# Optimization experiments

Hardware: AMD Instinct MI355X
Metric: run time of the kernel (lower is better)

## Reference

```python
import math
import jax, jax.numpy as jnp
import numpy as np
from jax.scipy.special import xlogy, gammaln

WINDOW = 256  # window_size from init_kwargs


def get_positional_embed(seq_len, feature_size):
    # Enformer-style relative positional features; feature_size % 6 == 0.
    distances = jnp.arange(-seq_len + 1, seq_len, dtype=jnp.float32)  # (2W-1,)
    nb = feature_size // 6
    absd = jnp.abs(distances)[:, None]  # (2W-1, 1)
    # exponential basis
    max_range = math.log(seq_len) / math.log(2.0)
    half_life = 2.0 ** jnp.linspace(3.0, max_range, nb)
    feat_exp = jnp.exp(-math.log(2.0) / half_life[None, :] * absd)
    # central mask basis
    center_widths = 2.0 ** jnp.arange(1, nb + 1, dtype=jnp.float32) - 1.0
    feat_cm = (center_widths[None, :] > absd).astype(jnp.float32)
    # gamma pdf basis
    stddev = seq_len / (2.0 * nb)
    start_mean = seq_len / nb
    mean = jnp.linspace(start_mean, float(seq_len), nb)[None, :]
    concentration = (mean / stddev) ** 2
    rate = mean / stddev ** 2
    log_unnorm = xlogy(concentration - 1.0, absd) - rate * absd
    log_norm = gammaln(concentration) - concentration * jnp.log(rate)
    prob = jnp.exp(log_unnorm - log_norm) + 1e-8
    feat_gamma = prob / jnp.max(prob, axis=-1, keepdims=True)
    emb = jnp.concatenate([feat_exp, feat_cm, feat_gamma], axis=-1)
    return jnp.concatenate([emb, jnp.sign(distances)[:, None] * emb], axis=-1)  # (2W-1, F)


def relative_shift_swin(x):
    # x: (b, h, nw, t1, t2) with t2 = 2*t1 - 1  ->  (b, h, nw, t1, t1)
    b, h, w, t1, t2 = x.shape
    x = jnp.pad(x, ((0, 0), (0, 0), (0, 0), (0, 0), (1, 0)))  # pad zero at front of last dim
    x = x.reshape(b, h, w, t2 + 1, t1)
    x = x[:, :, :, 1:, :].reshape(b, h, w, t1, t2)
    return x[..., :(t2 + 1) // 2]


def setup_inputs() -> dict:
    key = jax.random.key(0)
    ks = jax.random.split(key, 7)
    B, N, C, H, D = 2, 8192, 768, 12, 64
    return {
        "x": jax.random.normal(ks[0], (B, N, C), jnp.float32),
        "w_qkv": jax.random.normal(ks[1], (C, 3 * H * D), jnp.float32) * 0.02,
        "w_out": jax.random.normal(ks[2], (H * D, C), jnp.float32) * 0.02,
        "b_out": jnp.zeros((C,), jnp.float32),
        "w_rel": jax.random.normal(ks[3], (C, H * D), jnp.float32) * 0.02,
        "rel_content_bias": jax.random.normal(ks[4], (1, H, 1, 1, D), jnp.float32),
        "rel_pos_bias": jax.random.normal(ks[5], (1, H, 1, 1, D), jnp.float32),
    }


def reference(x, w_qkv, w_out, b_out, w_rel, rel_content_bias, rel_pos_bias):
    b, n, c = x.shape
    H, D = rel_content_bias.shape[1], rel_content_bias.shape[-1]
    W = WINDOW
    nw = n // W  # n divisible by W (no padding branch)
    # qkv projection; output layout of to_qkv is (h, d, k) per 'b n (h d k) -> k b h n d'
    qkv = (x @ w_qkv).reshape(b, n, H, D, 3)
    q = jnp.transpose(qkv[..., 0], (0, 2, 1, 3)).reshape(b, H, nw, W, D)
    k = jnp.transpose(qkv[..., 1], (0, 2, 1, 3)).reshape(b, H, nw, W, D)
    v = jnp.transpose(qkv[..., 2], (0, 2, 1, 3)).reshape(b, H, nw, W, D)
    # relative position keys: 'n (h d) -> h n d'
    F = w_rel.shape[0]
    positions = get_positional_embed(W, F)  # (2W-1, F)
    rel_k = jnp.transpose((positions @ w_rel).reshape(2 * W - 1, H, D), (1, 0, 2))  # (H, 2W-1, D)
    # content attention (scaled); position attention (unscaled, as in source)
    content_attn = jnp.einsum('bhwid,bhwjd->bhwij', q + rel_content_bias, k) * (D ** -0.5)
    rel_logits = jnp.einsum('bhwid,hjd->bhwij', q + rel_pos_bias, rel_k)  # (b,H,nw,W,2W-1)
    position_attn = relative_shift_swin(rel_logits)  # (b,H,nw,W,W)
    attn = jax.nn.softmax(content_attn + position_attn, axis=-1)
    out = jnp.einsum('bhwij,bhwjd->bhwid', attn, v)  # (b,H,nw,W,D)
    out = jnp.transpose(out, (0, 2, 3, 1, 4)).reshape(b, nw, W, H * D)  # 'b h w n d -> b w n (h d)'
    out = out @ w_out + b_out
    return out.reshape(b, n, c)
```

## Files before the change

kernel.cpp:

```cpp
#include <hip/hip_runtime.h>
#include <math.h>

typedef __attribute__((ext_vector_type(8))) short bf8;
typedef __attribute__((ext_vector_type(4))) float f4;
typedef __attribute__((ext_vector_type(2))) unsigned u2;
typedef __attribute__((ext_vector_type(4))) unsigned u4;

__device__ __forceinline__ float bf2f(short s) {
    union { unsigned u; float f; } v; v.u = ((unsigned)(unsigned short)s) << 16; return v.f;
}
__device__ __forceinline__ short f2bf(float f) {
    return (short)((__float_as_uint(f) + 0x8000u) >> 16);
}
__device__ __forceinline__ unsigned pk2(float a, float b) {
    unsigned ua = __float_as_uint(a) + 0x8000u;
    unsigned ub = __float_as_uint(b) + 0x8000u;
    return __builtin_amdgcn_perm(ub, ua, 0x07060302u);
}
__device__ __forceinline__ void gload16(const short* g, short* l) {
    __builtin_amdgcn_global_load_lds(
        (const __attribute__((address_space(1))) void*)g,
        (__attribute__((address_space(3))) void*)l,
        16, 0, 0);
}

__global__ __launch_bounds__(256) void xb_k(const float* __restrict__ X, short* __restrict__ XB) {
    long idx = (long)blockIdx.x * 256 + threadIdx.x;
    const float* src = X + idx * 8;
    float4 v0 = *(const float4*)(src);
    float4 v1 = *(const float4*)(src + 4);
    u4 p; p.x = pk2(v0.x, v0.y); p.y = pk2(v0.z, v0.w);
    p.z = pk2(v1.x, v1.y); p.w = pk2(v1.z, v1.w);
    *(u4*)(XB + idx * 8) = p;
}

__global__ void pos_kernel(short* __restrict__ P) {
    const int row = blockIdx.x;
    const int j = threadIdx.x;
    if (row == 511) {
        for (int t = j; t < 768; t += 128) P[511 * 768 + t] = 0;
        return;
    }
    const double dist = (double)(row - 255);
    const double ad = fabs(dist);
    double hl = exp2(3.0 + 5.0 * (double)j / 127.0);
    double fe = exp(-M_LN2 / hl * ad);
    double cw = exp2((double)(j + 1)) - 1.0;
    double fc = (cw > ad) ? 1.0 : 0.0;
    double m = 2.0 + 2.0 * (double)j;
    double conc = m * m;
    double lun = (ad == 0.0) ? -INFINITY : (conc - 1.0) * log(ad);
    lun -= m * ad;
    double lnorm = lgamma(conc) - conc * log(m);
    double prob = exp(lun - lnorm) + 1e-8;
    __shared__ double red[128];
    red[j] = prob;
    __syncthreads();
    for (int s2 = 64; s2 > 0; s2 >>= 1) {
        if (j < s2) red[j] = fmax(red[j], red[j + s2]);
        __syncthreads();
    }
    double fg = prob / red[0];
    float sg = (dist > 0.0) ? 1.f : ((dist < 0.0) ? -1.f : 0.f);
    int base = row * 768;
    P[base + j]        = f2bf((float)fe);
    P[base + 128 + j]  = f2bf((float)fc);
    P[base + 256 + j]  = f2bf((float)fg);
    P[base + 384 + j]  = f2bf(sg * (float)fe);
    P[base + 512 + j]  = f2bf(sg * (float)fc);
    P[base + 640 + j]  = f2bf(sg * (float)fg);
}

__global__ void wT_k(const float* __restrict__ W, short* __restrict__ WT,
                     int K, int N, int qperm) {
    int idx = blockIdx.x * 256 + threadIdx.x;
    int kq = K >> 2;
    if (idx >= N * kq) return;
    int n = idx / kq, k = (idx % kq) << 2;
    int rp = n;
    if (qperm) { int sel = n % 3, hd = n / 3; rp = sel * 768 + hd; }
    float a = W[(long)(k + 0) * N + n];
    float b = W[(long)(k + 1) * N + n];
    float c = W[(long)(k + 2) * N + n];
    float d = W[(long)(k + 3) * N + n];
    u2 r; r.x = pk2(a, b); r.y = pk2(c, d);
    *(u2*)(WT + (long)rp * K + k) = r;
}

__global__ __launch_bounds__(256) void gemm_k(
    const short* __restrict__ A, const short* __restrict__ BT,
    int M, int N, int K, int mode,
    short* __restrict__ Cb, float* __restrict__ Cf, const float* __restrict__ bias,
    short* __restrict__ Qo, short* __restrict__ Ko, short* __restrict__ Vt)
{
    __shared__ __attribute__((aligned(16))) short lds[2][8192];
    const int tid = threadIdx.x;
    const int lane = tid & 63;
    const int wave = tid >> 6;
    const int wm = wave >> 1, wn = wave & 1;
    const int c = lane & 15, quad = lane >> 4;
    const int m0 = blockIdx.x * 128, n0 = blockIdx.y * 128;
    const int lrow = lane >> 2;
    const int lslot = lane & 3;

    f4 acc[4][4];
#pragma unroll
    for (int i = 0; i < 4; ++i)
#pragma unroll
        for (int jx = 0; jx < 4; ++jx) acc[i][jx] = (f4){0.f, 0.f, 0.f, 0.f};

    const int nT = K >> 5;

    auto stage = [&](int buf, int k0) {
        short* As = &lds[buf][0];
        short* Bs = &lds[buf][4096];
#pragma unroll
        for (int i = 0; i < 2; ++i) {
            int grp = wave * 2 + i;
            int row = grp * 16 + lrow;
            int ss = lslot ^ ((row >> 1) & 3);
            const short* srcA;
            if (mode == 2) {
                int m = m0 + row;
                srcA = A + (((long)((m >> 13) * 12 + (k0 >> 6)) * 8192 + (m & 8191)) * 64
                            + (k0 & 63) + ss * 8);
            } else {
                srcA = A + (long)(m0 + row) * K + k0 + ss * 8;
            }
            gload16(srcA, &As[grp * 512]);
            const short* srcB = BT + (long)(n0 + row) * K + k0 + ss * 8;
            gload16(srcB, &Bs[grp * 512]);
        }
    };

    stage(0, 0);
    __syncthreads();

    for (int t = 0, cur = 0; t < nT; ++t, cur ^= 1) {
        if (t + 1 < nT) stage(cur ^ 1, (t + 1) << 5);
        const short* As = &lds[cur][0];
        const short* Bs = &lds[cur][4096];
        bf8 a[4], b[4];
#pragma unroll
        for (int mt = 0; mt < 4; ++mt) {
            int row = wm * 64 + mt * 16 + c;
            int slot = quad ^ ((row >> 1) & 3);
            a[mt] = *(const bf8*)(&As[row * 32 + slot * 8]);
        }
#pragma unroll
        for (int nt = 0; nt < 4; ++nt) {
            int row = wn * 64 + nt * 16 + c;
            int slot = quad ^ ((row >> 1) & 3);
            b[nt] = *(const bf8*)(&Bs[row * 32 + slot * 8]);
        }
#pragma unroll
        for (int mt = 0; mt < 4; ++mt)
#pragma unroll
            for (int nt = 0; nt < 4; ++nt)
                acc[mt][nt] = __builtin_amdgcn_mfma_f32_16x16x32_bf16(a[mt], b[nt], acc[mt][nt], 0, 0, 0);
        __syncthreads();
    }

    if (mode == 1) {
        const int sel = n0 / 768;
        if (sel == 2) {
#pragma unroll
            for (int mt = 0; mt < 4; ++mt)
#pragma unroll
                for (int nt = 0; nt < 4; ++nt)
#pragma unroll
                    for (int r = 0; r < 4; ++r) {
                        int m = m0 + wm * 64 + mt * 16 + quad * 4 + r;
                        int np = n0 - 1536 + wn * 64 + nt * 16 + c;
                        int h = np >> 6, d = np & 63;
                        int bb = m >> 13, nn = m & 8191;
                        long off = ((long)((bb * 12 + h) * 32 + (nn >> 8))) * 16384 + d * 256 + (nn & 255);
                        Vt[off] = f2bf(acc[mt][nt][r]);
                    }
        } else {
            short* dst = (sel == 0) ? Qo : Ko;
            const int nb = n0 - sel * 768;
#pragma unroll
            for (int mt = 0; mt < 4; ++mt)
#pragma unroll
                for (int nt = 0; nt < 4; ++nt)
#pragma unroll
                    for (int r = 0; r < 4; ++r) {
                        int m = m0 + wm * 64 + mt * 16 + quad * 4 + r;
                        int np = nb + wn * 64 + nt * 16 + c;
                        int h = np >> 6, d = np & 63;
                        int bb = m >> 13, nn = m & 8191;
                        long off = ((long)((bb * 12 + h) * 8192 + nn)) * 64 + d;
                        dst[off] = f2bf(acc[mt][nt][r]);
                    }
        }
    } else {
#pragma unroll
        for (int mt = 0; mt < 4; ++mt)
#pragma unroll
            for (int nt = 0; nt < 4; ++nt)
#pragma unroll
                for (int r = 0; r < 4; ++r) {
                    int m = m0 + wm * 64 + mt * 16 + quad * 4 + r;
                    int n = n0 + wn * 64 + nt * 16 + c;
                    float val = acc[mt][nt][r];
                    if (mode == 2) {
                        Cf[(long)m * N + n] = val + bias[n];
                    } else {
                        Cb[(long)m * N + n] = f2bf(val);
                    }
                }
    }
}

__global__ __launch_bounds__(256) void attn_k(
    short* __restrict__ Q, const short* __restrict__ Kk, const short* __restrict__ Vt,
    const short* __restrict__ RK,
    const float* __restrict__ rcb, const float* __restrict__ rpb)
{
    __shared__ __attribute__((aligned(16))) short Ks[256 * 64];
    __shared__ __attribute__((aligned(16))) short Ps[4][16 * 36];
    const int bid = blockIdx.x;
    const int low = bid & 7;
    const int wlo = low >> 1;
    const int hlo = low & 1;
    const int rest = bid >> 3;
    const int strip = rest & 3;
    const int t_ = rest >> 2;
    const int whi = t_ & 7;
    const int u_ = t_ >> 3;
    const int h = ((u_ % 6) << 1) | hlo;
    const int b = u_ / 6;
    const int w = (whi << 2) | wlo;
    const int tid = threadIdx.x, lane = tid & 63, wave = tid >> 6;
    const int c = lane & 15, quad = lane >> 4;
    const int i0w = strip * 64 + wave * 16;

    const long base_bh = ((long)(b * 12 + h) * 8192 + (long)w * 256) * 64;
    short* Qh = Q + base_bh;
    const short* Kh = Kk + base_bh;
    const short* Vw = Vt + (((long)(b * 12 + h) * 32 + w) << 14);
    const short* RKh = RK + h * 64;

#pragma unroll
    for (int i = 0; i < 8; ++i) {
        int p = tid + i * 256;
        int row = p >> 3, ls = p & 7;
        gload16(Kh + row * 64 + (ls ^ (row & 7)) * 8, &Ks[(wave * 64 + i * 256) * 8]);
    }

    bf8 qc[2], qp[2];
#pragma unroll
    for (int ks = 0; ks < 2; ++ks) {
        bf8 qraw = *(const bf8*)(Qh + (i0w + c) * 64 + ks * 32 + quad * 8);
        float4 cb0 = *(const float4*)(rcb + h * 64 + ks * 32 + quad * 8);
        float4 cb1 = *(const float4*)(rcb + h * 64 + ks * 32 + quad * 8 + 4);
        float4 pb0 = *(const float4*)(rpb + h * 64 + ks * 32 + quad * 8);
        float4 pb1 = *(const float4*)(rpb + h * 64 + ks * 32 + quad * 8 + 4);
        float cbv[8] = {cb0.x, cb0.y, cb0.z, cb0.w, cb1.x, cb1.y, cb1.z, cb1.w};
        float pbv[8] = {pb0.x, pb0.y, pb0.z, pb0.w, pb1.x, pb1.y, pb1.z, pb1.w};
#pragma unroll
        for (int u = 0; u < 8; ++u) {
            float qv = bf2f(qraw[u]);
            qc[ks][u] = f2bf(qv + cbv[u]);
            qp[ks][u] = f2bf(qv + pbv[u]);
        }
    }
    __syncthreads();

    f4 S[16];
#pragma unroll
    for (int ct = 0; ct < 16; ++ct) S[ct] = (f4){0.f, 0.f, 0.f, 0.f};
#pragma unroll
    for (int t = 0; t < 16; ++t) {
        int row = t * 16 + c;
#pragma unroll
        for (int ks = 0; ks < 2; ++ks) {
            bf8 kf = *(const bf8*)(&Ks[row * 64 + (((ks * 4 + quad) ^ (row & 7))) * 8]);
            S[t] = __builtin_amdgcn_mfma_f32_16x16x32_bf16(qc[ks], kf, S[t], 0, 0, 0);
        }
    }
    __syncthreads();

    short* Vs = Ks;
#pragma unroll
    for (int i = 0; i < 8; ++i) {
        int p = tid + i * 256;
        int row = p >> 5, ls = p & 31;
        gload16(Vw + row * 256 + (ls ^ ((row & 7) << 2)) * 8, &Vs[(wave * 2 + i * 8) * 256]);
    }

    const int r0 = 240 - i0w;
    int src_[4];
#pragma unroll
    for (int r = 0; r < 4; ++r) {
        int ip = quad * 4 + r;
        src_[r] = (lane & 48) | ((15 - ip + c) & 15);
    }
    float rotp[4], rotc[4];
#pragma unroll
    for (int t = 0; t < 17; ++t) {
        bf8 rf0 = *(const bf8*)(RKh + (long)(r0 + t * 16 + c) * 768 + quad * 8);
        bf8 rf1 = *(const bf8*)(RKh + (long)(r0 + t * 16 + c) * 768 + 32 + quad * 8);
        f4 Rt = (f4){0.f, 0.f, 0.f, 0.f};
        Rt = __builtin_amdgcn_mfma_f32_16x16x32_bf16(qp[0], rf0, Rt, 0, 0, 0);
        Rt = __builtin_amdgcn_mfma_f32_16x16x32_bf16(qp[1], rf1, Rt, 0, 0, 0);
#pragma unroll
        for (int r = 0; r < 4; ++r) rotc[r] = __shfl(Rt[r], src_[r]);
        if (t > 0) {
#pragma unroll
            for (int r = 0; r < 4; ++r) {
                int ip = quad * 4 + r;
                float pos = (c <= ip) ? rotp[r] : rotc[r];
                S[t - 1][r] = S[t - 1][r] * 0.125f + pos;
            }
        }
#pragma unroll
        for (int r = 0; r < 4; ++r) rotp[r] = rotc[r];
    }

    float mx[4] = {-3.4e38f, -3.4e38f, -3.4e38f, -3.4e38f};
#pragma unroll
    for (int ct = 0; ct < 16; ++ct)
#pragma unroll
        for (int r = 0; r < 4; ++r) mx[r] = fmaxf(mx[r], S[ct][r]);
#pragma unroll
    for (int r = 0; r < 4; ++r)
#pragma unroll
        for (int o = 1; o < 16; o <<= 1) mx[r] = fmaxf(mx[r], __shfl_xor(mx[r], o));
    float sm[4] = {0.f, 0.f, 0.f, 0.f};
#pragma unroll
    for (int ct = 0; ct < 16; ++ct)
#pragma unroll
        for (int r = 0; r < 4; ++r) {
            float p = __expf(S[ct][r] - mx[r]);
            S[ct][r] = p;
            sm[r] += p;
        }
#pragma unroll
    for (int r = 0; r < 4; ++r)
#pragma unroll
        for (int o = 1; o < 16; o <<= 1) sm[r] += __shfl_xor(sm[r], o);
    float inv[4];
#pragma unroll
    for (int r = 0; r < 4; ++r) inv[r] = 1.0f / sm[r];

    __syncthreads();

    f4 O[4];
#pragma unroll
    for (int vt = 0; vt < 4; ++vt) O[vt] = (f4){0.f, 0.f, 0.f, 0.f};
#pragma unroll
    for (int kt = 0; kt < 8; ++kt) {
#pragma unroll
        for (int r = 0; r < 4; ++r) {
            Ps[wave][(quad * 4 + r) * 36 + c]      = f2bf(S[kt * 2][r] * inv[r]);
            Ps[wave][(quad * 4 + r) * 36 + 16 + c] = f2bf(S[kt * 2 + 1][r] * inv[r]);
        }
        bf8 af = *(const bf8*)(&Ps[wave][c * 36 + quad * 8]);
#pragma unroll
        for (int vt = 0; vt < 4; ++vt) {
            int row = vt * 16 + c;
            int slot = ((kt * 4 + quad) ^ ((row & 7) << 2));
            bf8 bv = *(const bf8*)(&Vs[row * 256 + slot * 8]);
            O[vt] = __builtin_amdgcn_mfma_f32_16x16x32_bf16(af, bv, O[vt], 0, 0, 0);
        }
    }
#pragma unroll
    for (int vt = 0; vt < 4; ++vt)
#pragma unroll
        for (int r = 0; r < 4; ++r)
            Qh[(i0w + quad * 4 + r) * 64 + vt * 16 + c] = f2bf(O[vt][r]);
}

extern "C" void kernel_launch(void* const* d_in, const int* in_sizes, int n_in,
                              void* d_out, int out_size, void* d_ws, size_t ws_size,
                              hipStream_t stream) {
    const float* x     = (const float*)d_in[0];
    const float* w_qkv = (const float*)d_in[1];
    const float* w_out = (const float*)d_in[2];
    const float* b_out = (const float*)d_in[3];
    const float* w_rel = (const float*)d_in[4];
    const float* rcb   = (const float*)d_in[5];
    const float* rpb   = (const float*)d_in[6];

    char* ws = (char*)d_ws;
    short* wqkvT = (short*)(ws);
    short* woutT = (short*)(ws + 3538944L);
    short* wrelT = (short*)(ws + 4718592L);
    short* pos   = (short*)(ws + 5898240L);
    short* relk  = (short*)(ws + 6684672L);
    short* q     = (short*)(ws + 7471104L);
    short* k     = (short*)(ws + 32636928L);
    short* vT    = (short*)(ws + 57802752L);
    short* xb    = (short*)d_out;

    wT_k<<<(2304 * 192 + 255) / 256, 256, 0, stream>>>(w_qkv, wqkvT, 768, 2304, 1);
    wT_k<<<(768 * 192 + 255) / 256, 256, 0, stream>>>(w_out, woutT, 768, 768, 0);
    wT_k<<<(768 * 192 + 255) / 256, 256, 0, stream>>>(w_rel, wrelT, 768, 768, 0);
    pos_kernel<<<512, 128, 0, stream>>>(pos);
    xb_k<<<6144, 256, 0, stream>>>(x, xb);
    gemm_k<<<dim3(4, 6), 256, 0, stream>>>(pos, wrelT, 512, 768, 768, 0,
                                           relk, nullptr, nullptr, nullptr, nullptr, nullptr);
    gemm_k<<<dim3(128, 18), 256, 0, stream>>>(xb, wqkvT, 16384, 2304, 768, 1,
                                              nullptr, nullptr, nullptr, q, k, vT);
    attn_k<<<3072, 256, 0, stream>>>(q, k, vT, relk, rcb, rpb);
    gemm_k<<<dim3(128, 6), 256, 0, stream>>>(q, woutT, 16384, 768, 768, 2,
                                             nullptr, (float*)d_out, b_out, nullptr, nullptr, nullptr);
}
```

Baseline: 332.3 us.

## Add 256x256-tile 8-wave GEMM with 4-stage async LDS pipeline for QKV/out projections

Introduces a new GEMM kernel with 512 threads and 256x256 output tiles, each wave computing 128x64. It uses a 4-slot LDS ring filled by direct global-to-LDS loads with explicit vmcnt waits and raised priority around the MFMA block. Both the QKV and output projections switch to it. The intent is more operand reuse and less load latency exposure, at the cost of 128KB of LDS per block (likely one block per CU) and fewer blocks to spread across CUs.

```diff
diff --git a/kernel.cpp b/kernel.cpp
--- a/kernel.cpp
+++ b/kernel.cpp
@@ -161,16 +161,114 @@
         __syncthreads();
     }
 
+#pragma unroll
+    for (int mt = 0; mt < 4; ++mt)
+#pragma unroll
+        for (int nt = 0; nt < 4; ++nt)
+#pragma unroll
+            for (int r = 0; r < 4; ++r) {
+                int m = m0 + wm * 64 + mt * 16 + quad * 4 + r;
+                int n = n0 + wn * 64 + nt * 16 + c;
+                float val = acc[mt][nt][r];
+                if (mode == 2) {
+                    Cf[(long)m * N + n] = val + bias[n];
+                } else {
+                    Cb[(long)m * N + n] = f2bf(val);
+                }
+            }
+}
+
+__global__ __launch_bounds__(512) void gemm8_k(
+    const short* __restrict__ A, const short* __restrict__ BT,
+    int M, int N, int K, int mode,
+    float* __restrict__ Cf, const float* __restrict__ bias,
+    short* __restrict__ Qo, short* __restrict__ Ko, short* __restrict__ Vt)
+{
+    __shared__ __attribute__((aligned(16))) short L[4][16384];
+    const int tid = threadIdx.x;
+    const int lane = tid & 63;
+    const int wave = tid >> 6;
+    const int wm = wave >> 2, wn = wave & 3;
+    const int c = lane & 15, quad = lane >> 4;
+    const int m0 = blockIdx.x * 256, n0 = blockIdx.y * 256;
+    const int lrow = lane >> 2;
+    const int lslot = lane & 3;
+
+    f4 acc[8][4];
+#pragma unroll
+    for (int i = 0; i < 8; ++i)
+#pragma unroll
+        for (int jx = 0; jx < 4; ++jx) acc[i][jx] = (f4){0.f, 0.f, 0.f, 0.f};
+
+    const int nT = K >> 5;
+
+    auto stage = [&](int t) {
+        int slot = t & 3;
+        int k0 = t << 5;
+#pragma unroll
+        for (int i = 0; i < 2; ++i) {
+            int row = i * 128 + wave * 16 + lrow;
+            int ss = lslot ^ ((row >> 1) & 3);
+            const short* srcA;
+            if (mode == 2) {
+                int m = m0 + row;
+                srcA = A + (((long)((m >> 13) * 12 + (k0 >> 6)) * 8192 + (m & 8191)) * 64
+                            + (k0 & 63) + ss * 8);
+            } else {
+                srcA = A + (long)(m0 + row) * K + k0 + ss * 8;
+            }
+            gload16(srcA, &L[slot][i * 4096 + wave * 512]);
+            const short* srcB = BT + (long)(n0 + row) * K + k0 + ss * 8;
+            gload16(srcB, &L[slot][8192 + i * 4096 + wave * 512]);
+        }
+    };
+
+    stage(0); stage(1); stage(2);
+
+#define KSTEP(T, NVSTR, DO_STAGE)                                              \
+    {                                                                          \
+        if (DO_STAGE) stage((T) + 3);                                          \
+        asm volatile("s_waitcnt vmcnt(" NVSTR ")" ::: "memory");               \
+        asm volatile("s_barrier" ::: "memory");                                \
+        const short* As = &L[(T) & 3][0];                                      \
+        const short* Bs = &L[(T) & 3][8192];                                   \
+        bf8 a_[8], b_[4];                                                      \
+        _Pragma("unroll")                                                      \
+        for (int nt = 0; nt < 4; ++nt) {                                       \
+            int row = wn * 64 + nt * 16 + c;                                   \
+            b_[nt] = *(const bf8*)(&Bs[row * 32 + (quad ^ ((row >> 1) & 3)) * 8]); \
+        }                                                                      \
+        _Pragma("unroll")                                                      \
+        for (int mt = 0; mt < 8; ++mt) {                                       \
+            int row = wm * 128 + mt * 16 + c;                                  \
+            a_[mt] = *(const bf8*)(&As[row * 32 + (quad ^ ((row >> 1) & 3)) * 8]); \
+        }                                                                      \
+        __builtin_amdgcn_s_setprio(1);                                         \
+        _Pragma("unroll")                                                      \
+        for (int mt = 0; mt < 8; ++mt)                                         \
+            _Pragma("unroll")                                                  \
+            for (int nt = 0; nt < 4; ++nt)                                     \
+                acc[mt][nt] = __builtin_amdgcn_mfma_f32_16x16x32_bf16(a_[mt], b_[nt], acc[mt][nt], 0, 0, 0); \
+        __builtin_amdgcn_s_setprio(0);                                         \
+        asm volatile("s_barrier" ::: "memory");                                \
+    }
+
+    for (int t = 0; t < nT - 3; ++t) KSTEP(t, "12", true);
+    KSTEP(nT - 3, "8", false);
+    KSTEP(nT - 2, "4", false);
+    KSTEP(nT - 1, "0", false);
+#undef KSTEP
+
     if (mode == 1) {
         const int sel = n0 / 768;
         if (sel == 2) {
 #pragma unroll
-            for (int mt = 0; mt < 4; ++mt)
+            for (int mt = 0; mt < 8; ++mt)
 #pragma unroll
                 for (int nt = 0; nt < 4; ++nt)
 #pragma unroll
                     for (int r = 0; r < 4; ++r) {
-                        int m = m0 + wm * 64 + mt * 16 + quad * 4 + r;
+                        int m = m0 + wm * 128 + mt * 16 + quad * 4 + r;
                         int np = n0 - 1536 + wn * 64 + nt * 16 + c;
                         int h = np >> 6, d = np & 63;
                         int bb = m >> 13, nn = m & 8191;
@@ -181,12 +279,12 @@
             short* dst = (sel == 0) ? Qo : Ko;
             const int nb = n0 - sel * 768;
 #pragma unroll
-            for (int mt = 0; mt < 4; ++mt)
+            for (int mt = 0; mt < 8; ++mt)
 #pragma unroll
                 for (int nt = 0; nt < 4; ++nt)
 #pragma unroll
                     for (int r = 0; r < 4; ++r) {
-                        int m = m0 + wm * 64 + mt * 16 + quad * 4 + r;
+                        int m = m0 + wm * 128 + mt * 16 + quad * 4 + r;
                         int np = nb + wn * 64 + nt * 16 + c;
                         int h = np >> 6, d = np & 63;
                         int bb = m >> 13, nn = m & 8191;
@@ -196,19 +294,14 @@
         }
     } else {
 #pragma unroll
-        for (int mt = 0; mt < 4; ++mt)
+        for (int mt = 0; mt < 8; ++mt)
 #pragma unroll
             for (int nt = 0; nt < 4; ++nt)
 #pragma unroll
                 for (int r = 0; r < 4; ++r) {
-                    int m = m0 + wm * 64 + mt * 16 + quad * 4 + r;
+                    int m = m0 + wm * 128 + mt * 16 + quad * 4 + r;
                     int n = n0 + wn * 64 + nt * 16 + c;
-                    float val = acc[mt][nt][r];
-                    if (mode == 2) {
-                        Cf[(long)m * N + n] = val + bias[n];
-                    } else {
-                        Cb[(long)m * N + n] = f2bf(val);
-                    }
+                    Cf[(long)m * N + n] = acc[mt][nt][r] + bias[n];
                 }
     }
 }
@@ -402,9 +495,9 @@
     xb_k<<<6144, 256, 0, stream>>>(x, xb);
     gemm_k<<<dim3(4, 6), 256, 0, stream>>>(pos, wrelT, 512, 768, 768, 0,
                                            relk, nullptr, nullptr, nullptr, nullptr, nullptr);
-    gemm_k<<<dim3(128, 18), 256, 0, stream>>>(xb, wqkvT, 16384, 2304, 768, 1,
-                                              nullptr, nullptr, nullptr, q, k, vT);
+    gemm8_k<<<dim3(64, 9), 512, 0, stream>>>(xb, wqkvT, 16384, 2304, 768, 1,
+                                             nullptr, nullptr, q, k, vT);
     attn_k<<<3072, 256, 0, stream>>>(q, k, vT, relk, rcb, rpb);
-    gemm_k<<<dim3(128, 6), 256, 0, stream>>>(q, woutT, 16384, 768, 768, 2,
-                                             nullptr, (float*)d_out, b_out, nullptr, nullptr, nullptr);
-}
+    gemm8_k<<<dim3(64, 3), 512, 0, stream>>>(q, woutT, 16384, 768, 768, 2,
+                                             (float*)d_out, b_out, nullptr, nullptr, nullptr);
+}
```

Measured after the change: 341.9 us. 1.03x slower.

## Triple-buffer GEMM LDS staging with explicit vmcnt waits

Applied to the files above, without the earlier changes.

Changes the GEMM's LDS staging from double to triple buffering. Global-to-LDS loads are issued two k-steps ahead, and explicit s_waitcnt vmcnt counts with raw s_barrier replace __syncthreads, so more load latency can overlap with MFMA work. LDS use per block rises to 48KB, which may lower occupancy, and correctness now depends on the vmcnt counts matching the number of loads issued per stage (4 per thread).

```diff
diff --git a/kernel.cpp b/kernel.cpp
--- a/kernel.cpp
+++ b/kernel.cpp
@@ -93,7 +93,7 @@
     short* __restrict__ Cb, float* __restrict__ Cf, const float* __restrict__ bias,
     short* __restrict__ Qo, short* __restrict__ Ko, short* __restrict__ Vt)
 {
-    __shared__ __attribute__((aligned(16))) short lds[2][8192];
+    __shared__ __attribute__((aligned(16))) short L[3][8192];
     const int tid = threadIdx.x;
     const int lane = tid & 63;
     const int wave = tid >> 6;
@@ -111,9 +111,10 @@
 
     const int nT = K >> 5;
 
-    auto stage = [&](int buf, int k0) {
-        short* As = &lds[buf][0];
-        short* Bs = &lds[buf][4096];
+    auto stage = [&](int t) {
+        short* As = &L[t % 3][0];
+        short* Bs = &L[t % 3][4096];
+        int k0 = t << 5;
 #pragma unroll
         for (int i = 0; i < 2; ++i) {
             int grp = wave * 2 + i;
@@ -133,13 +134,20 @@
         }
     };
 
-    stage(0, 0);
-    __syncthreads();
-
-    for (int t = 0, cur = 0; t < nT; ++t, cur ^= 1) {
-        if (t + 1 < nT) stage(cur ^ 1, (t + 1) << 5);
-        const short* As = &lds[cur][0];
-        const short* Bs = &lds[cur][4096];
+    stage(0); stage(1);
+
+    for (int t = 0; t < nT; ++t) {
+        if (t + 2 < nT) {
+            stage(t + 2);
+            asm volatile("s_waitcnt vmcnt(8)" ::: "memory");
+        } else if (t + 1 < nT) {
+            asm volatile("s_waitcnt vmcnt(4)" ::: "memory");
+        } else {
+            asm volatile("s_waitcnt vmcnt(0)" ::: "memory");
+        }
+        asm volatile("s_barrier" ::: "memory");
+        const short* As = &L[t % 3][0];
+        const short* Bs = &L[t % 3][4096];
         bf8 a[4], b[4];
 #pragma unroll
         for (int mt = 0; mt < 4; ++mt) {
@@ -158,7 +166,7 @@
 #pragma unroll
             for (int nt = 0; nt < 4; ++nt)
                 acc[mt][nt] = __builtin_amdgcn_mfma_f32_16x16x32_bf16(a[mt], b[nt], acc[mt][nt], 0, 0, 0);
-        __syncthreads();
+        asm volatile("s_barrier" ::: "memory");
     }
 
     if (mode == 1) {
```

New measurement: 332.6 us. About the same (+0.1%).
